# Kernel tuning notes

Measured on AMD Instinct MI355X. Metric: run time of the kernel, lower is better.

## Reference

```python
import jax, jax.numpy as jnp
import numpy as np
import math

B, L, D = 8, 1024, 1024
H = 16
NS = 8
HD = D // H

def setup_inputs() -> dict:
    key = jax.random.key(0)
    ks = jax.random.split(key, 9)
    s = 1.0 / math.sqrt(D)
    inp = {
        "x": jax.random.normal(ks[0], (B, L, D), dtype=jnp.float32),
        "key_padding_mask": jnp.ones((B, L), dtype=bool),
        "Wq_s": jax.random.normal(ks[1], (D, D), dtype=jnp.float32) * s,
        "Wk_s": jax.random.normal(ks[2], (D, D), dtype=jnp.float32) * s,
        "Wv_s": jax.random.normal(ks[3], (D, D), dtype=jnp.float32) * s,
        "Wq_ns": jax.random.normal(ks[4], (NS, D, D), dtype=jnp.float32) * s,
        "Wk_ns": jax.random.normal(ks[5], (NS, D, D), dtype=jnp.float32) * s,
        "Wv_ns": jax.random.normal(ks[6], (NS, D, D), dtype=jnp.float32) * s,
        "W_out": jax.random.normal(ks[7], (D, D), dtype=jnp.float32) * s,
    }
    return inp

def _mixed_proj(x, W_shared, W_ns):
    # x: [B, L, D]; W_shared: [D, D] (out,in); W_ns: [NS, D, D] (per-position out,in)
    L_s = x.shape[1] - W_ns.shape[0]
    s_proj = jnp.einsum('bld,ed->ble', x[:, :L_s], W_shared)       # shared prefix
    ns_proj = jnp.einsum('bnd,ned->bne', x[:, L_s:], W_ns)          # per-position tail
    return jnp.concatenate([s_proj, ns_proj], axis=1)

def reference(x, key_padding_mask, Wq_s, Wk_s, Wv_s, Wq_ns, Wk_ns, Wv_ns, W_out):
    Bv, Lv, Dv = x.shape
    q = _mixed_proj(x, Wq_s, Wq_ns)  # query_len=None -> full
    k = _mixed_proj(x, Wk_s, Wk_ns)
    v = _mixed_proj(x, Wv_s, Wv_ns)
    # [B, H, L, HD]
    q = q.reshape(Bv, Lv, H, HD).transpose(0, 2, 1, 3)
    k = k.reshape(Bv, Lv, H, HD).transpose(0, 2, 1, 3)
    v = v.reshape(Bv, Lv, H, HD).transpose(0, 2, 1, 3)
    causal = jnp.tril(jnp.ones((Lv, Lv), dtype=bool))               # [L_q, L_k]
    mask = causal[None, :, :] & key_padding_mask[:, None, :]        # [B, L_q, L_k]
    scores = jnp.einsum('bhqd,bhkd->bhqk', q, k) / math.sqrt(HD)
    scores = jnp.where(mask[:, None, :, :], scores, jnp.float32(-1e9))
    attn = jax.nn.softmax(scores, axis=-1)  # dropout is identity in eval
    out = jnp.einsum('bhqk,bhkd->bhqd', attn, v)
    out = out.transpose(0, 2, 1, 3).reshape(Bv, Lv, Dv)
    return jnp.einsum('bld,ed->ble', out, W_out)
```

## Files before the change

### kernel.cpp

```cpp
#include <hip/hip_runtime.h>

#define Bsz  8
#define Lsz  1024
#define Dsz  1024
#define Hh   16
#define HDsz 64
#define NSsz 8
#define LSsz 1016

typedef short  bf16x8 __attribute__((ext_vector_type(8)));
typedef float  f32x4  __attribute__((ext_vector_type(4)));

#define GLB(p) ((const __attribute__((address_space(1))) unsigned int*)(p))
#define LDSP(p) ((__attribute__((address_space(3))) unsigned int*)(p))

__device__ __forceinline__ float bf2f(unsigned short u) {
    union { unsigned int i; float f; } v; v.i = ((unsigned int)u) << 16; return v.f;
}
__device__ __forceinline__ unsigned short f2bf(float f) {
    union { float f; unsigned int i; } v; v.f = f;
    unsigned int x = v.i;
    return (unsigned short)((x + 0x7FFFu + ((x >> 16) & 1u)) >> 16);
}
__device__ __forceinline__ void gload(const unsigned short* g, unsigned short* l) {
    __builtin_amdgcn_global_load_lds(GLB(g), LDSP(l), 16, 0, 0);
}

__global__ __launch_bounds__(256) void cast_kernel(
    const float* __restrict__ x,
    const float* __restrict__ wq, const float* __restrict__ wk,
    const float* __restrict__ wv, const float* __restrict__ wo,
    unsigned short* __restrict__ xb,
    unsigned short* __restrict__ wcat,
    unsigned short* __restrict__ wob)
{
    const size_t NX = 2097152;
    const size_t NW = 262144;
    size_t i = (size_t)blockIdx.x * 256 + threadIdx.x;
    const size_t stride = (size_t)gridDim.x * 256;
    const size_t total = NX + 4 * NW;
    for (; i < total; i += stride) {
        const float* src; unsigned short* dst; size_t off;
        if (i < NX)               { src = x;  dst = xb;             off = i; }
        else if (i < NX + NW)     { src = wq; dst = wcat;           off = i - NX; }
        else if (i < NX + 2 * NW) { src = wk; dst = wcat + 1048576; off = i - NX - NW; }
        else if (i < NX + 3 * NW) { src = wv; dst = wcat + 2097152; off = i - NX - 2 * NW; }
        else                      { src = wo; dst = wob;            off = i - NX - 3 * NW; }
        float4 v = reinterpret_cast<const float4*>(src)[off];
        ushort4 o;
        o.x = f2bf(v.x); o.y = f2bf(v.y); o.z = f2bf(v.z); o.w = f2bf(v.w);
        reinterpret_cast<ushort4*>(dst)[off] = o;
    }
}

template <bool C_F32, bool SPLIT>
__global__ __launch_bounds__(512, 2) void gemm8_kernel(
    const unsigned short* __restrict__ Ab,
    const unsigned short* __restrict__ Wb,
    void* __restrict__ O0, void* __restrict__ O1, void* __restrict__ O2)
{
    __shared__ __align__(16) unsigned short As[3 * 16384];
    __shared__ __align__(16) unsigned short Bs[3 * 8192];

    const int tid  = threadIdx.x;
    const int lane = tid & 63;
    const int wave = tid >> 6;
    const int wm   = wave >> 2;
    const int wn   = wave & 3;
    const int lr   = lane & 15;
    const int lq   = lane >> 4;
    const int m0   = blockIdx.y * 256;
    const int n0   = blockIdx.x * 128;

    const int srow = tid >> 3;
    const int sc8  = tid & 7;

    auto stage_ph = [&](int tt, int ph) {
        const int k0 = tt * 64;
        unsigned short* Abase = &As[(tt % 3) * 16384];
        unsigned short* Bbase = &Bs[(tt % 3) * 8192];
        if (ph == 0) {
            #pragma unroll
            for (int u = 0; u < 2; ++u) {
                int r = u * 64 + srow;
                int c = sc8 ^ (r & 7);
                gload(&Ab[(size_t)(m0 + r) * 1024 + k0 + c * 8],
                      &Abase[u * 4096 + wave * 512]);
            }
            int r = srow, c = sc8 ^ (r & 7);
            gload(&Wb[(size_t)(n0 + r) * 1024 + k0 + c * 8],
                  &Bbase[wave * 512]);
        } else {
            #pragma unroll
            for (int u = 2; u < 4; ++u) {
                int r = u * 64 + srow;
                int c = sc8 ^ (r & 7);
                gload(&Ab[(size_t)(m0 + r) * 1024 + k0 + c * 8],
                      &Abase[u * 4096 + wave * 512]);
            }
            int r = 64 + srow, c = sc8 ^ (r & 7);
            gload(&Wb[(size_t)(n0 + r) * 1024 + k0 + c * 8],
                  &Bbase[4096 + wave * 512]);
        }
    };

    f32x4 acc[8][2];
    #pragma unroll
    for (int i = 0; i < 8; ++i)
        #pragma unroll
        for (int j = 0; j < 2; ++j)
            acc[i][j] = (f32x4){0.f, 0.f, 0.f, 0.f};

    stage_ph(0, 0); stage_ph(0, 1);
    stage_ph(1, 0); stage_ph(1, 1);
    asm volatile("s_waitcnt vmcnt(6)" ::: "memory");
    __builtin_amdgcn_s_barrier();

    for (int t = 0; t < 16; ++t) {
        const unsigned short* Abuf = &As[(t % 3) * 16384];
        const unsigned short* Bbuf = &Bs[(t % 3) * 8192];
        #pragma unroll
        for (int ks = 0; ks < 2; ++ks) {
            bf16x8 af[8], bfr[2];
            #pragma unroll
            for (int i = 0; i < 8; ++i) {
                int row = wm * 128 + i * 16 + lr;
                af[i] = *reinterpret_cast<const bf16x8*>(
                    &Abuf[row * 64 + (((ks * 4 + lq) ^ (row & 7)) << 3)]);
            }
            #pragma unroll
            for (int j = 0; j < 2; ++j) {
                int row = wn * 32 + j * 16 + lr;
                bfr[j] = *reinterpret_cast<const bf16x8*>(
                    &Bbuf[row * 64 + (((ks * 4 + lq) ^ (row & 7)) << 3)]);
            }
            if (t + 2 < 16) stage_ph(t + 2, ks);
            if (ks == 1) {
                if (t + 2 < 16)
                    asm volatile("s_waitcnt vmcnt(6)" ::: "memory");
                else if (t + 1 < 16)
                    asm volatile("s_waitcnt vmcnt(0)" ::: "memory");
            }
            __builtin_amdgcn_s_barrier();
            asm volatile("s_waitcnt lgkmcnt(0)" ::: "memory");
            __builtin_amdgcn_sched_barrier(0);
            __builtin_amdgcn_s_setprio(1);
            #pragma unroll
            for (int i = 0; i < 8; ++i)
                #pragma unroll
                for (int j = 0; j < 2; ++j)
                    acc[i][j] = __builtin_amdgcn_mfma_f32_16x16x32_bf16(
                        af[i], bfr[j], acc[i][j], 0, 0, 0);
            __builtin_amdgcn_s_setprio(0);
            __builtin_amdgcn_s_barrier();
        }
    }

    if (SPLIT) {
        const int tsel = n0 >> 10;
        const int d0   = n0 & 1023;
        unsigned short* Out =
            (unsigned short*)(tsel == 0 ? O0 : tsel == 1 ? O1 : O2);
        #pragma unroll
        for (int i = 0; i < 8; ++i)
            #pragma unroll
            for (int j = 0; j < 2; ++j) {
                int col = d0 + wn * 32 + j * 16 + lr;
                #pragma unroll
                for (int r = 0; r < 4; ++r) {
                    int row = m0 + wm * 128 + i * 16 + lq * 4 + r;
                    Out[(size_t)row * 1024 + col] = f2bf(acc[i][j][r]);
                }
            }
    } else {
        float* Co = (float*)O0;
        #pragma unroll
        for (int i = 0; i < 8; ++i)
            #pragma unroll
            for (int j = 0; j < 2; ++j) {
                int col = n0 + wn * 32 + j * 16 + lr;
                #pragma unroll
                for (int r = 0; r < 4; ++r) {
                    int row = m0 + wm * 128 + i * 16 + lq * 4 + r;
                    Co[(size_t)row * 1024 + col] = acc[i][j][r];
                }
            }
    }
}

#define GBM 128
#define GBN 128
#define GBK 64

template <bool A_F32, bool C_F32>
__global__ __launch_bounds__(256) void gemm_bt_kernel(
    const void* __restrict__ Av,
    const float* __restrict__ W,
    void* __restrict__ Cv,
    int M, int N, int K)
{
    __shared__ unsigned short As[GBM][GBK];
    __shared__ unsigned short Ws[GBN][GBK];

    const int tid  = threadIdx.x;
    const int lane = tid & 63;
    const int wave = tid >> 6;
    const int wm   = wave >> 1;
    const int wn   = wave & 1;
    const int lr   = lane & 15;
    const int lq   = lane >> 4;
    const int m0   = blockIdx.y * GBM;
    const int n0   = blockIdx.x * GBN;

    f32x4 acc[4][4];
    #pragma unroll
    for (int i = 0; i < 4; ++i)
        #pragma unroll
        for (int j = 0; j < 4; ++j)
            acc[i][j] = (f32x4){0.f, 0.f, 0.f, 0.f};

    for (int k0 = 0; k0 < K; k0 += GBK) {
        if (A_F32) {
            const float* A = (const float*)Av;
            #pragma unroll
            for (int i = 0; i < 8; ++i) {
                int idx = tid + i * 256;
                int row = idx >> 4;
                int c4  = idx & 15;
                float4 a = *reinterpret_cast<const float4*>(
                    &A[(size_t)(m0 + row) * K + k0 + c4 * 4]);
                ushort4 o;
                o.x = f2bf(a.x); o.y = f2bf(a.y);
                o.z = f2bf(a.z); o.w = f2bf(a.w);
                *reinterpret_cast<ushort4*>(&As[row][c4 * 4]) = o;
            }
        } else {
            const unsigned short* A = (const unsigned short*)Av;
            #pragma unroll
            for (int i = 0; i < 4; ++i) {
                int idx = tid + i * 256;
                int row = idx >> 3;
                int c8  = idx & 7;
                int4 v = *reinterpret_cast<const int4*>(
                    &A[(size_t)(m0 + row) * K + k0 + c8 * 8]);
                *reinterpret_cast<int4*>(&As[row][c8 * 8]) = v;
            }
        }
        #pragma unroll
        for (int i = 0; i < 8; ++i) {
            int idx = tid + i * 256;
            int row = idx >> 4;
            int c4  = idx & 15;
            float4 w = *reinterpret_cast<const float4*>(
                &W[(size_t)(n0 + row) * K + k0 + c4 * 4]);
            ushort4 o;
            o.x = f2bf(w.x); o.y = f2bf(w.y);
            o.z = f2bf(w.z); o.w = f2bf(w.w);
            *reinterpret_cast<ushort4*>(&Ws[row][c4 * 4]) = o;
        }
        __syncthreads();

        #pragma unroll
        for (int ks = 0; ks < 2; ++ks) {
            bf16x8 af[4], bfr[4];
            #pragma unroll
            for (int i = 0; i < 4; ++i)
                af[i] = *reinterpret_cast<const bf16x8*>(
                    &As[wm * 64 + i * 16 + lr][ks * 32 + lq * 8]);
            #pragma unroll
            for (int j = 0; j < 4; ++j)
                bfr[j] = *reinterpret_cast<const bf16x8*>(
                    &Ws[wn * 64 + j * 16 + lr][ks * 32 + lq * 8]);
            #pragma unroll
            for (int i = 0; i < 4; ++i)
                #pragma unroll
                for (int j = 0; j < 4; ++j)
                    acc[i][j] = __builtin_amdgcn_mfma_f32_16x16x32_bf16(
                        af[i], bfr[j], acc[i][j], 0, 0, 0);
        }
        __syncthreads();
    }

    #pragma unroll
    for (int i = 0; i < 4; ++i) {
        #pragma unroll
        for (int j = 0; j < 4; ++j) {
            int col = n0 + wn * 64 + j * 16 + lr;
            #pragma unroll
            for (int r = 0; r < 4; ++r) {
                int row = m0 + wm * 64 + i * 16 + lq * 4 + r;
                if (C_F32) {
                    ((float*)Cv)[(size_t)row * N + col] = acc[i][j][r];
                } else {
                    ((unsigned short*)Cv)[(size_t)row * N + col] = f2bf(acc[i][j][r]);
                }
            }
        }
    }
}

__global__ __launch_bounds__(512) void fixup_kernel(
    const float* __restrict__ x,
    const float* __restrict__ Wq_ns,
    const float* __restrict__ Wk_ns,
    const float* __restrict__ Wv_ns,
    unsigned short* __restrict__ Q,
    unsigned short* __restrict__ Kb,
    unsigned short* __restrict__ V)
{
    const int bid   = blockIdx.x;
    const int wgt   = bid >> 6;
    const int chunk = bid & 63;
    const int proj  = wgt >> 3;
    const int n     = wgt & 7;
    const float* Wns =
        (proj == 0 ? Wq_ns : proj == 1 ? Wk_ns : Wv_ns) + (size_t)n * Dsz * Dsz;
    unsigned short* Out = (proj == 0 ? Q : proj == 1 ? Kb : V);
    const int l    = LSsz + n;
    const int b    = threadIdx.x >> 6;
    const int lane = threadIdx.x & 63;

    const float* xrow = x + ((size_t)b * Lsz + l) * Dsz;
    float4 xr[4];
    #pragma unroll
    for (int i = 0; i < 4; ++i)
        xr[i] = *reinterpret_cast<const float4*>(&xrow[lane * 4 + i * 256]);

    for (int er = 0; er < 16; ++er) {
        const int e = chunk * 16 + er;
        const float* wrow = Wns + (size_t)e * Dsz;
        float s = 0.f;
        #pragma unroll
        for (int i = 0; i < 4; ++i) {
            float4 wv = *reinterpret_cast<const float4*>(&wrow[lane * 4 + i * 256]);
            s += wv.x * xr[i].x + wv.y * xr[i].y
               + wv.z * xr[i].z + wv.w * xr[i].w;
        }
        #pragma unroll
        for (int off = 32; off > 0; off >>= 1) s += __shfl_xor(s, off, 64);
        if (lane == 0) Out[((size_t)b * Lsz + l) * Dsz + e] = f2bf(s);
    }
}

__global__ __launch_bounds__(256, 4) void attn_mfma_kernel(
    const unsigned short* __restrict__ Q,
    const unsigned short* __restrict__ K,
    const unsigned short* __restrict__ V,
    unsigned short* __restrict__ O)
{
    __shared__ __align__(16) unsigned short Klds[2 * 4096];
    __shared__ __align__(16) unsigned short Vtlds[4096];
    __shared__ __align__(16) unsigned short Plds[4][1024];

    const int tid  = threadIdx.x;
    const int lane = tid & 63;
    const int wave = tid >> 6;
    const int lr   = lane & 15;
    const int lq   = lane >> 4;

    const int id = blockIdx.x;
    const int qt = 15 - ((id >> 3) & 15);
    const int bh = ((id >> 7) << 3) | (id & 7);
    const int h  = bh & (Hh - 1);
    const int b  = bh >> 4;
    const int qw = qt * 64 + wave * 16;
    const int nkt = qt + 1;

    const size_t base = (size_t)b * Lsz * Dsz + (size_t)h * HDsz;

    bf16x8 qf[2];
    #pragma unroll
    for (int h2 = 0; h2 < 2; ++h2) {
        bf16x8 t = *reinterpret_cast<const bf16x8*>(
            &Q[base + (size_t)(qw + lr) * Dsz + h2 * 32 + lq * 8]);
        #pragma unroll
        for (int e = 0; e < 8; ++e) {
            float f = bf2f((unsigned short)t[e]) * 0.125f;
            t[e] = (short)f2bf(f);
        }
        qf[h2] = t;
    }

    f32x4 acc[4];
    #pragma unroll
    for (int jd = 0; jd < 4; ++jd) acc[jd] = (f32x4){0.f, 0.f, 0.f, 0.f};
    float m_i[4] = {-1e30f, -1e30f, -1e30f, -1e30f};
    float l_i[4] = {0.f, 0.f, 0.f, 0.f};

    const int krow0 = tid >> 3;
    const int kc8   = tid & 7;
    const int vd0   = (tid & 7) * 8;
    const int vk0   = (tid >> 3) * 2;

    unsigned short* Pw = &Plds[wave][0];
    int4 vq0, vq1;

    #pragma unroll
    for (int it = 0; it < 2; ++it) {
        int row  = it * 32 + krow0;
        int csrc = kc8 ^ (row & 7);
        const unsigned short* ga = &K[base + (size_t)row * Dsz + csrc * 8];
        __builtin_amdgcn_global_load_lds(GLB(ga),
            LDSP(&Klds[it * 2048 + wave * 512]), 16, 0, 0);
    }
    vq0 = *reinterpret_cast<const int4*>(&V[base + (size_t)(vk0 + 0) * Dsz + vd0]);
    vq1 = *reinterpret_cast<const int4*>(&V[base + (size_t)(vk0 + 1) * Dsz + vd0]);

    for (int kt = 0; kt < nkt; ++kt) {
        const int k0 = kt * 64;
        const int kb = (kt & 1) * 4096;

        __syncthreads();

        {
            union { int4 v; unsigned short u[8]; } a, c;
            a.v = vq0; c.v = vq1;
            const int kc  = vk0 >> 3;
            const int klo = vk0 & 7;
            #pragma unroll
            for (int d = 0; d < 8; ++d) {
                int dd  = vd0 + d;
                int idx = dd * 64 + (((kc ^ (dd & 7)) << 3) | klo);
                ushort2 p; p.x = a.u[d]; p.y = c.u[d];
                *reinterpret_cast<ushort2*>(&Vtlds[idx]) = p;
            }
        }
        __syncthreads();

        if (kt + 1 < nkt) {
            const int k0n = k0 + 64;
            #pragma unroll
            for (int it = 0; it < 2; ++it) {
                int row  = it * 32 + krow0;
                int csrc = kc8 ^ (row & 7);
                const unsigned short* ga =
                    &K[base + (size_t)(k0n + row) * Dsz + csrc * 8];
                __builtin_amdgcn_global_load_lds(GLB(ga),
                    LDSP(&Klds[(kb ^ 4096) + it * 2048 + wave * 512]), 16, 0, 0);
            }
            vq0 = *reinterpret_cast<const int4*>(
                &V[base + (size_t)(k0n + vk0 + 0) * Dsz + vd0]);
            vq1 = *reinterpret_cast<const int4*>(
                &V[base + (size_t)(k0n + vk0 + 1) * Dsz + vd0]);
        }

        f32x4 sv[4];
        #pragma unroll
        for (int jt = 0; jt < 4; ++jt) sv[jt] = (f32x4){0.f, 0.f, 0.f, 0.f};

        __builtin_amdgcn_s_setprio(1);
        #pragma unroll
        for (int h2 = 0; h2 < 2; ++h2) {
            const int cs = (((h2 << 2) | lq) ^ (lr & 7)) << 3;
            #pragma unroll
            for (int jt = 0; jt < 4; ++jt) {
                bf16x8 kf = *reinterpret_cast<const bf16x8*>(
                    &Klds[kb + (jt * 16 + lr) * 64 + cs]);
                sv[jt] = __builtin_amdgcn_mfma_f32_16x16x32_bf16(
                    qf[h2], kf, sv[jt], 0, 0, 0);
            }
        }
        __builtin_amdgcn_s_setprio(0);

        if (k0 + 63 > qw) {
            #pragma unroll
            for (int jt = 0; jt < 4; ++jt) {
                int kpos = k0 + jt * 16 + lr;
                #pragma unroll
                for (int r = 0; r < 4; ++r) {
                    int q = qw + lq * 4 + r;
                    if (kpos > q) sv[jt][r] = -1e30f;
                }
            }
        }

        float tm[4], al[4], rs[4];
        #pragma unroll
        for (int r = 0; r < 4; ++r)
            tm[r] = fmaxf(fmaxf(sv[0][r], sv[1][r]), fmaxf(sv[2][r], sv[3][r]));
        #pragma unroll
        for (int off = 1; off < 16; off <<= 1)
            #pragma unroll
            for (int r = 0; r < 4; ++r)
                tm[r] = fmaxf(tm[r], __shfl_xor(tm[r], off, 64));
        #pragma unroll
        for (int r = 0; r < 4; ++r) {
            float nm = fmaxf(m_i[r], tm[r]);
            al[r] = __expf(m_i[r] - nm);
            m_i[r] = nm;
        }
        #pragma unroll
        for (int jt = 0; jt < 4; ++jt)
            #pragma unroll
            for (int r = 0; r < 4; ++r)
                sv[jt][r] = __expf(sv[jt][r] - m_i[r]);
        #pragma unroll
        for (int r = 0; r < 4; ++r)
            rs[r] = (sv[0][r] + sv[1][r]) + (sv[2][r] + sv[3][r]);
        #pragma unroll
        for (int off = 1; off < 16; off <<= 1)
            #pragma unroll
            for (int r = 0; r < 4; ++r)
                rs[r] += __shfl_xor(rs[r], off, 64);
        #pragma unroll
        for (int r = 0; r < 4; ++r) l_i[r] = l_i[r] * al[r] + rs[r];
        #pragma unroll
        for (int jd = 0; jd < 4; ++jd)
            #pragma unroll
            for (int r = 0; r < 4; ++r)
                acc[jd][r] *= al[r];

        #pragma unroll
        for (int jt = 0; jt < 4; ++jt) {
            int kcol  = jt * 16 + lr;
            int chunk = kcol >> 3;
            int elem  = kcol & 7;
            #pragma unroll
            for (int r = 0; r < 4; ++r) {
                int qrow = lq * 4 + r;
                Pw[qrow * 64 + (((chunk ^ (qrow & 7)) << 3) | elem)] =
                    f2bf(sv[jt][r]);
            }
        }

        __builtin_amdgcn_s_setprio(1);
        #pragma unroll
        for (int h2 = 0; h2 < 2; ++h2) {
            const int cs = (((h2 << 2) | lq) ^ (lr & 7)) << 3;
            bf16x8 pf = *reinterpret_cast<const bf16x8*>(&Pw[lr * 64 + cs]);
            #pragma unroll
            for (int jd = 0; jd < 4; ++jd) {
                bf16x8 vf = *reinterpret_cast<const bf16x8*>(
                    &Vtlds[(jd * 16 + lr) * 64 + cs]);
                acc[jd] = __builtin_amdgcn_mfma_f32_16x16x32_bf16(
                    pf, vf, acc[jd], 0, 0, 0);
            }
        }
        __builtin_amdgcn_s_setprio(0);
    }

    float inv[4];
    #pragma unroll
    for (int r = 0; r < 4; ++r) inv[r] = 1.0f / l_i[r];
    #pragma unroll
    for (int jd = 0; jd < 4; ++jd) {
        #pragma unroll
        for (int r = 0; r < 4; ++r) {
            int qrow  = lq * 4 + r;
            int col   = jd * 16 + lr;
            int chunk = col >> 3;
            int elem  = col & 7;
            Pw[qrow * 64 + (((chunk ^ (qrow & 7)) << 3) | elem)] =
                f2bf(acc[jd][r] * inv[r]);
        }
    }
    #pragma unroll
    for (int it2 = 0; it2 < 2; ++it2) {
        int row = it2 * 8 + (lane >> 3);
        int c   = lane & 7;
        const int4 ov = *reinterpret_cast<const int4*>(
            &Pw[row * 64 + ((c ^ (row & 7)) << 3)]);
        *reinterpret_cast<int4*>(&O[base + (size_t)(qw + row) * Dsz + c * 8]) = ov;
    }
}

extern "C" void kernel_launch(void* const* d_in, const int* in_sizes, int n_in,
                              void* d_out, int out_size, void* d_ws, size_t ws_size,
                              hipStream_t stream)
{
    const float* x     = (const float*)d_in[0];
    const float* Wq_s  = (const float*)d_in[2];
    const float* Wk_s  = (const float*)d_in[3];
    const float* Wv_s  = (const float*)d_in[4];
    const float* Wq_ns = (const float*)d_in[5];
    const float* Wk_ns = (const float*)d_in[6];
    const float* Wv_ns = (const float*)d_in[7];
    const float* W_out = (const float*)d_in[8];
    float* out = (float*)d_out;

    const size_t nElem = (size_t)Bsz * Lsz * Dsz;
    unsigned short* Q    = (unsigned short*)d_ws;
    unsigned short* Kb   = Q + nElem;
    unsigned short* V    = Kb + nElem;
    unsigned short* Xb   = V + nElem;
    unsigned short* Wcat = Xb + nElem;
    unsigned short* Wob  = Wcat + 3 * 1048576;
    const size_t need = (4 * nElem + 4 * 1048576) * sizeof(unsigned short);

    if (ws_size >= need) {
        cast_kernel<<<3072, 256, 0, stream>>>(x, Wq_s, Wk_s, Wv_s, W_out,
                                              Xb, Wcat, Wob);
        gemm8_kernel<false, true><<<dim3(24, 32), 512, 0, stream>>>(
            Xb, Wcat, Q, Kb, V);
        fixup_kernel<<<24 * 64, 512, 0, stream>>>(x, Wq_ns, Wk_ns, Wv_ns, Q, Kb, V);
        unsigned short* O = Xb;
        attn_mfma_kernel<<<Bsz * Hh * (Lsz / 64), 256, 0, stream>>>(Q, Kb, V, O);
        gemm8_kernel<true, false><<<dim3(8, 32), 512, 0, stream>>>(
            O, Wob, out, nullptr, nullptr);
    } else {
        unsigned short* O = Xb;
        dim3 ggrid(Dsz / GBN, (Bsz * Lsz) / GBM);
        gemm_bt_kernel<true, false><<<ggrid, 256, 0, stream>>>(x, Wq_s, Q,  Bsz * Lsz, Dsz, Dsz);
        gemm_bt_kernel<true, false><<<ggrid, 256, 0, stream>>>(x, Wk_s, Kb, Bsz * Lsz, Dsz, Dsz);
        gemm_bt_kernel<true, false><<<ggrid, 256, 0, stream>>>(x, Wv_s, V,  Bsz * Lsz, Dsz, Dsz);
        fixup_kernel<<<24 * 64, 512, 0, stream>>>(x, Wq_ns, Wk_ns, Wv_ns, Q, Kb, V);
        attn_mfma_kernel<<<Bsz * Hh * (Lsz / 64), 256, 0, stream>>>(Q, Kb, V, O);
        gemm_bt_kernel<false, true><<<ggrid, 256, 0, stream>>>(O, W_out, out, Bsz * Lsz, Dsz, Dsz);
    }
}
```

Baseline: 369.8 us.

## Replace GEMM with double-buffered 128x128 tile kernel, add lazy softmax rescale

The 256x128 triple-buffered 8-wave GEMM becomes a 128x128, 4-wave, double-buffered kernel. It uses a 1D grid with an XCD-aware block swizzle, loads both k-substeps before running the MFMAs, and has one barrier per k-tile. Separately, the attention kernel skips the online-softmax rescale of the accumulator and row sum unless some row maximum grows by more than 8, which cuts exp and multiply work. The fixup loop also gets an unroll hint. The changes trade fewer barriers and better L2 locality against less prefetch depth and possible exp-range risk from stale maxima.

```diff
diff --git a/kernel.cpp b/kernel.cpp
--- a/kernel.cpp
+++ b/kernel.cpp
@@ -54,106 +54,93 @@
 }
 
 template <bool C_F32, bool SPLIT>
-__global__ __launch_bounds__(512, 2) void gemm8_kernel(
+__global__ __launch_bounds__(256, 2) void gemm2ph_kernel(
     const unsigned short* __restrict__ Ab,
     const unsigned short* __restrict__ Wb,
+    int NB,
     void* __restrict__ O0, void* __restrict__ O1, void* __restrict__ O2)
 {
-    __shared__ __align__(16) unsigned short As[3 * 16384];
-    __shared__ __align__(16) unsigned short Bs[3 * 8192];
+    __shared__ __align__(16) unsigned short As[2][8192];
+    __shared__ __align__(16) unsigned short Bs[2][8192];
 
     const int tid  = threadIdx.x;
     const int lane = tid & 63;
     const int wave = tid >> 6;
-    const int wm   = wave >> 2;
-    const int wn   = wave & 3;
+    const int wm   = wave >> 1;
+    const int wn   = wave & 1;
     const int lr   = lane & 15;
     const int lq   = lane >> 4;
-    const int m0   = blockIdx.y * 256;
-    const int n0   = blockIdx.x * 128;
-
-    const int srow = tid >> 3;
-    const int sc8  = tid & 7;
-
-    auto stage_ph = [&](int tt, int ph) {
-        const int k0 = tt * 64;
-        unsigned short* Abase = &As[(tt % 3) * 16384];
-        unsigned short* Bbase = &Bs[(tt % 3) * 8192];
-        if (ph == 0) {
-            #pragma unroll
-            for (int u = 0; u < 2; ++u) {
-                int r = u * 64 + srow;
-                int c = sc8 ^ (r & 7);
-                gload(&Ab[(size_t)(m0 + r) * 1024 + k0 + c * 8],
-                      &Abase[u * 4096 + wave * 512]);
-            }
-            int r = srow, c = sc8 ^ (r & 7);
+
+    const int cpx = gridDim.x >> 3;
+    const int fid = blockIdx.x;
+    const int swz = (fid & 7) * cpx + (fid >> 3);
+    const int nb  = swz % NB;
+    const int mb  = swz / NB;
+    const int m0  = mb * 128;
+    const int n0  = nb * 128;
+
+    const int srw = lane >> 3;
+    const int sc8 = lane & 7;
+
+    auto STAGE = [&](int t, int buf) {
+        const int k0 = t * 64;
+        #pragma unroll
+        for (int u = 0; u < 4; ++u) {
+            int r = u * 32 + wave * 8 + srw;
+            int c = sc8 ^ (r & 7);
+            gload(&Ab[(size_t)(m0 + r) * 1024 + k0 + c * 8],
+                  &As[buf][u * 2048 + wave * 512]);
             gload(&Wb[(size_t)(n0 + r) * 1024 + k0 + c * 8],
-                  &Bbase[wave * 512]);
-        } else {
-            #pragma unroll
-            for (int u = 2; u < 4; ++u) {
-                int r = u * 64 + srow;
-                int c = sc8 ^ (r & 7);
-                gload(&Ab[(size_t)(m0 + r) * 1024 + k0 + c * 8],
-                      &Abase[u * 4096 + wave * 512]);
-            }
-            int r = 64 + srow, c = sc8 ^ (r & 7);
-            gload(&Wb[(size_t)(n0 + r) * 1024 + k0 + c * 8],
-                  &Bbase[4096 + wave * 512]);
+                  &Bs[buf][u * 2048 + wave * 512]);
         }
     };
 
-    f32x4 acc[8][2];
-    #pragma unroll
-    for (int i = 0; i < 8; ++i)
-        #pragma unroll
-        for (int j = 0; j < 2; ++j)
+    f32x4 acc[4][4];
+    #pragma unroll
+    for (int i = 0; i < 4; ++i)
+        #pragma unroll
+        for (int j = 0; j < 4; ++j)
             acc[i][j] = (f32x4){0.f, 0.f, 0.f, 0.f};
 
-    stage_ph(0, 0); stage_ph(0, 1);
-    stage_ph(1, 0); stage_ph(1, 1);
-    asm volatile("s_waitcnt vmcnt(6)" ::: "memory");
+    STAGE(0, 0);
+    asm volatile("s_waitcnt vmcnt(0)" ::: "memory");
     __builtin_amdgcn_s_barrier();
 
+    int buf = 0;
     for (int t = 0; t < 16; ++t) {
-        const unsigned short* Abuf = &As[(t % 3) * 16384];
-        const unsigned short* Bbuf = &Bs[(t % 3) * 8192];
+        if (t + 1 < 16) STAGE(t + 1, buf ^ 1);
+
+        bf16x8 af[2][4], bfr[2][4];
         #pragma unroll
         for (int ks = 0; ks < 2; ++ks) {
-            bf16x8 af[8], bfr[2];
-            #pragma unroll
-            for (int i = 0; i < 8; ++i) {
-                int row = wm * 128 + i * 16 + lr;
-                af[i] = *reinterpret_cast<const bf16x8*>(
-                    &Abuf[row * 64 + (((ks * 4 + lq) ^ (row & 7)) << 3)]);
-            }
-            #pragma unroll
-            for (int j = 0; j < 2; ++j) {
-                int row = wn * 32 + j * 16 + lr;
-                bfr[j] = *reinterpret_cast<const bf16x8*>(
-                    &Bbuf[row * 64 + (((ks * 4 + lq) ^ (row & 7)) << 3)]);
-            }
-            if (t + 2 < 16) stage_ph(t + 2, ks);
-            if (ks == 1) {
-                if (t + 2 < 16)
-                    asm volatile("s_waitcnt vmcnt(6)" ::: "memory");
-                else if (t + 1 < 16)
-                    asm volatile("s_waitcnt vmcnt(0)" ::: "memory");
-            }
-            __builtin_amdgcn_s_barrier();
-            asm volatile("s_waitcnt lgkmcnt(0)" ::: "memory");
-            __builtin_amdgcn_sched_barrier(0);
-            __builtin_amdgcn_s_setprio(1);
-            #pragma unroll
-            for (int i = 0; i < 8; ++i)
+            #pragma unroll
+            for (int i = 0; i < 4; ++i) {
+                int row = wm * 64 + i * 16 + lr;
+                af[ks][i] = *reinterpret_cast<const bf16x8*>(
+                    &As[buf][row * 64 + (((ks * 4 + lq) ^ (row & 7)) << 3)]);
+            }
+            #pragma unroll
+            for (int j = 0; j < 4; ++j) {
+                int row = wn * 64 + j * 16 + lr;
+                bfr[ks][j] = *reinterpret_cast<const bf16x8*>(
+                    &Bs[buf][row * 64 + (((ks * 4 + lq) ^ (row & 7)) << 3)]);
+            }
+        }
+        asm volatile("s_waitcnt lgkmcnt(0)" ::: "memory");
+        __builtin_amdgcn_sched_barrier(0);
+        __builtin_amdgcn_s_setprio(1);
+        #pragma unroll
+        for (int ks = 0; ks < 2; ++ks)
+            #pragma unroll
+            for (int i = 0; i < 4; ++i)
                 #pragma unroll
-                for (int j = 0; j < 2; ++j)
+                for (int j = 0; j < 4; ++j)
                     acc[i][j] = __builtin_amdgcn_mfma_f32_16x16x32_bf16(
-                        af[i], bfr[j], acc[i][j], 0, 0, 0);
-            __builtin_amdgcn_s_setprio(0);
-            __builtin_amdgcn_s_barrier();
-        }
+                        af[ks][i], bfr[ks][j], acc[i][j], 0, 0, 0);
+        __builtin_amdgcn_s_setprio(0);
+        if (t + 1 < 16) asm volatile("s_waitcnt vmcnt(0)" ::: "memory");
+        __builtin_amdgcn_s_barrier();
+        buf ^= 1;
     }
 
     if (SPLIT) {
@@ -162,26 +149,26 @@
         unsigned short* Out =
             (unsigned short*)(tsel == 0 ? O0 : tsel == 1 ? O1 : O2);
         #pragma unroll
-        for (int i = 0; i < 8; ++i)
-            #pragma unroll
-            for (int j = 0; j < 2; ++j) {
-                int col = d0 + wn * 32 + j * 16 + lr;
+        for (int i = 0; i < 4; ++i)
+            #pragma unroll
+            for (int j = 0; j < 4; ++j) {
+                int col = d0 + wn * 64 + j * 16 + lr;
                 #pragma unroll
                 for (int r = 0; r < 4; ++r) {
-                    int row = m0 + wm * 128 + i * 16 + lq * 4 + r;
+                    int row = m0 + wm * 64 + i * 16 + lq * 4 + r;
                     Out[(size_t)row * 1024 + col] = f2bf(acc[i][j][r]);
                 }
             }
     } else {
         float* Co = (float*)O0;
         #pragma unroll
-        for (int i = 0; i < 8; ++i)
-            #pragma unroll
-            for (int j = 0; j < 2; ++j) {
-                int col = n0 + wn * 32 + j * 16 + lr;
+        for (int i = 0; i < 4; ++i)
+            #pragma unroll
+            for (int j = 0; j < 4; ++j) {
+                int col = n0 + wn * 64 + j * 16 + lr;
                 #pragma unroll
                 for (int r = 0; r < 4; ++r) {
-                    int row = m0 + wm * 128 + i * 16 + lq * 4 + r;
+                    int row = m0 + wm * 64 + i * 16 + lq * 4 + r;
                     Co[(size_t)row * 1024 + col] = acc[i][j][r];
                 }
             }
@@ -326,6 +313,7 @@
     for (int i = 0; i < 4; ++i)
         xr[i] = *reinterpret_cast<const float4*>(&xrow[lane * 4 + i * 256]);
 
+    #pragma unroll 4
     for (int er = 0; er < 16; ++er) {
         const int e = chunk * 16 + er;
         const float* wrow = Wns + (size_t)e * Dsz;
@@ -474,7 +462,7 @@
             }
         }
 
-        float tm[4], al[4], rs[4];
+        float tm[4];
         #pragma unroll
         for (int r = 0; r < 4; ++r)
             tm[r] = fmaxf(fmaxf(sv[0][r], sv[1][r]), fmaxf(sv[2][r], sv[3][r]));
@@ -483,12 +471,23 @@
             #pragma unroll
             for (int r = 0; r < 4; ++r)
                 tm[r] = fmaxf(tm[r], __shfl_xor(tm[r], off, 64));
-        #pragma unroll
-        for (int r = 0; r < 4; ++r) {
-            float nm = fmaxf(m_i[r], tm[r]);
-            al[r] = __expf(m_i[r] - nm);
-            m_i[r] = nm;
-        }
+
+        float dm = fmaxf(fmaxf(tm[0] - m_i[0], tm[1] - m_i[1]),
+                         fmaxf(tm[2] - m_i[2], tm[3] - m_i[3]));
+        if (!__all(dm <= 8.0f)) {
+            #pragma unroll
+            for (int r = 0; r < 4; ++r) {
+                float nm = fmaxf(m_i[r], tm[r]);
+                float al = __expf(m_i[r] - nm);
+                m_i[r] = nm;
+                l_i[r] *= al;
+                #pragma unroll
+                for (int jd = 0; jd < 4; ++jd)
+                    acc[jd][r] *= al;
+            }
+        }
+
+        float rs[4];
         #pragma unroll
         for (int jt = 0; jt < 4; ++jt)
             #pragma unroll
@@ -503,12 +502,7 @@
             for (int r = 0; r < 4; ++r)
                 rs[r] += __shfl_xor(rs[r], off, 64);
         #pragma unroll
-        for (int r = 0; r < 4; ++r) l_i[r] = l_i[r] * al[r] + rs[r];
-        #pragma unroll
-        for (int jd = 0; jd < 4; ++jd)
-            #pragma unroll
-            for (int r = 0; r < 4; ++r)
-                acc[jd][r] *= al[r];
+        for (int r = 0; r < 4; ++r) l_i[r] += rs[r];
 
         #pragma unroll
         for (int jt = 0; jt < 4; ++jt) {
@@ -590,13 +584,13 @@
     if (ws_size >= need) {
         cast_kernel<<<3072, 256, 0, stream>>>(x, Wq_s, Wk_s, Wv_s, W_out,
                                               Xb, Wcat, Wob);
-        gemm8_kernel<false, true><<<dim3(24, 32), 512, 0, stream>>>(
-            Xb, Wcat, Q, Kb, V);
+        gemm2ph_kernel<false, true><<<1536, 256, 0, stream>>>(
+            Xb, Wcat, 24, Q, Kb, V);
         fixup_kernel<<<24 * 64, 512, 0, stream>>>(x, Wq_ns, Wk_ns, Wv_ns, Q, Kb, V);
         unsigned short* O = Xb;
         attn_mfma_kernel<<<Bsz * Hh * (Lsz / 64), 256, 0, stream>>>(Q, Kb, V, O);
-        gemm8_kernel<true, false><<<dim3(8, 32), 512, 0, stream>>>(
-            O, Wob, out, nullptr, nullptr);
+        gemm2ph_kernel<true, false><<<512, 256, 0, stream>>>(
+            O, Wob, 8, out, nullptr, nullptr);
     } else {
         unsigned short* O = Xb;
         dim3 ggrid(Dsz / GBN, (Bsz * Lsz) / GBM);
```

Result: no change. 366.6 us (-0.9%).
